# Kernel tuning notes

Hardware: AMD Instinct MI355X
Metric: run time of the kernel (lower is better)

Reference implementation:

```python
import jax, jax.numpy as jnp
import numpy as np

INPUT_SIZE = 1024
OUTPUT_SIZE = 1024
HEADS = 8
FREQ = 10000.0
NEG_INF = -1e9


def absolute_position(T, d, freq):
    # AP[p, 2i] = sin(p / freq^(2i/d)); AP[p, 2i+1] = cos(...). T assumed even.
    pos = jnp.arange(T, dtype=jnp.float32)[:, None]          # [T, 1]
    i = jnp.arange(T // 2, dtype=jnp.float32)[None, :]       # [1, T//2]
    angle = pos / (freq ** (2.0 * i / d))                    # [T, T//2]
    return jnp.stack([jnp.sin(angle), jnp.cos(angle)], axis=-1).reshape(T, T)


def setup_inputs() -> dict:
    key = jax.random.key(0)
    k_x, k_m, k_q, k_k, k_v, k_o = jax.random.split(key, 6)
    bs, n = 4, 2048
    dh = OUTPUT_SIZE // HEADS
    s_in = 1.0 / np.sqrt(INPUT_SIZE)
    s_out = 1.0 / np.sqrt(OUTPUT_SIZE)
    return {
        "x": jax.random.normal(k_x, (bs, n, INPUT_SIZE), dtype=jnp.float32),
        "mask": jax.random.randint(k_m, (bs, n), 0, 2, dtype=jnp.int32),
        # torch Linear weight layout: [out_features, in_features], stacked per head -> [H, dh, D]
        "Wq": jax.random.uniform(k_q, (HEADS, dh, INPUT_SIZE), jnp.float32, -s_in, s_in),
        "Wk": jax.random.uniform(k_k, (HEADS, dh, INPUT_SIZE), jnp.float32, -s_in, s_in),
        "Wv": jax.random.uniform(k_v, (HEADS, dh, INPUT_SIZE), jnp.float32, -s_in, s_in),
        "Wout": jax.random.uniform(k_o, (INPUT_SIZE, OUTPUT_SIZE), jnp.float32, -s_out, s_out),
    }


def reference(x, mask, Wq, Wk, Wv, Wout):
    bs, n, d = x.shape
    # per-head projections (no bias): [b, h, n, dh]
    Q = jnp.einsum('bnd,hed->bhne', x, Wq)
    K = jnp.einsum('bnd,hed->bhne', x, Wk)
    V = jnp.einsum('bnd,hed->bhne', x, Wv)
    # unscaled scores, as in the original module
    energies = jnp.einsum('bhqe,bhke->bhqk', Q, K)             # [b, h, n, n]
    AP = absolute_position(n, d, FREQ)                         # [n, n]
    energies = energies + AP
    m = mask.astype(bool)
    attn_mask = m[:, None, :, None] & m[:, None, None, :]      # [b, 1, n, n]
    energies = jnp.where(attn_mask, energies, NEG_INF)
    A = jax.nn.softmax(energies, axis=-1)                      # [b, h, n, n]
    # original computes (V^T @ A)^T == A^T @ V  (note transposed attention)
    y = jnp.einsum('bhji,bhje->bhie', A, V)                    # [b, h, n, dh]
    y = y.transpose(0, 2, 1, 3).reshape(bs, n, -1)             # concat heads -> [b, n, D]
    out = jnp.einsum('bnd,od->bno', y, Wout)
    return out, A[:, -1]  # original returns last head's att_weights
```

## Files before the change

### kernel.cpp

```cpp
#include <hip/hip_runtime.h>
#include <math.h>

#define BS_ 4
#define N_  2048
#define D_  1024
#define H_  8
#define DH_ 128

typedef __attribute__((ext_vector_type(8))) short short8;
typedef __attribute__((ext_vector_type(4))) short short4_t;
typedef __attribute__((ext_vector_type(4))) float float4_t;
typedef unsigned short u16;

__device__ __forceinline__ u16 f2bf(float f) {
    union { float f; unsigned u; } v; v.f = f;
    unsigned r = v.u + 0x7FFFu + ((v.u >> 16) & 1u);
    return (u16)(r >> 16);
}
__device__ __forceinline__ float bf2f(u16 h) {
    union { unsigned u; float f; } v; v.u = ((unsigned)h) << 16;
    return v.f;
}
__device__ __forceinline__ void split4(float a, float b, float c, float d,
                                       short4_t* hi, short4_t* lo) {
    u16 h0 = f2bf(a), h1 = f2bf(b), h2 = f2bf(c), h3 = f2bf(d);
    (*hi)[0] = (short)h0; (*hi)[1] = (short)h1; (*hi)[2] = (short)h2; (*hi)[3] = (short)h3;
    (*lo)[0] = (short)f2bf(a - bf2f(h0));
    (*lo)[1] = (short)f2bf(b - bf2f(h1));
    (*lo)[2] = (short)f2bf(c - bf2f(h2));
    (*lo)[3] = (short)f2bf(d - bf2f(h3));
}

__device__ __forceinline__ void gl_lds16(const void* g, void* l) {
    __builtin_amdgcn_global_load_lds(
        (const __attribute__((address_space(1))) unsigned int*)g,
        (__attribute__((address_space(3))) unsigned int*)l,
        16, 0, 0);
}

__global__ void apt_kernel(unsigned int* __restrict__ APtw) {
    int idx = blockIdx.x * 256 + threadIdx.x;
    int i = idx >> 10;
    int jw = idx & 1023;
    int u = i >> 1;
    float ex = exp2f(-(float)u * (13.287712379549449f / 512.0f));
    float a0 = (float)(2 * jw) * ex;
    float a1 = (float)(2 * jw + 1) * ex;
    float v0, v1;
    if (i & 1) { v0 = cosf(a0); v1 = cosf(a1); }
    else       { v0 = sinf(a0); v1 = sinf(a1); }
    APtw[(size_t)i * (N_ / 2) + jw] = (unsigned)f2bf(v0) | ((unsigned)f2bf(v1) << 16);
}

__global__ void split_kernel(const float* __restrict__ x,
                             const float* __restrict__ Wq, const float* __restrict__ Wk,
                             const float* __restrict__ Wv, const float* __restrict__ Wo,
                             u16* __restrict__ Xhi, u16* __restrict__ Xlo,
                             u16* __restrict__ Whi, u16* __restrict__ Wlo,
                             u16* __restrict__ Wvhi, u16* __restrict__ Wohi) {
    int i = blockIdx.x * 256 + threadIdx.x;
    const float* src; u16 *dhi, *dlo; size_t off;
    if (i < 2097152)      { src = x  + 4*(size_t)i;             dhi = Xhi;  dlo = Xlo;  off = 4*(size_t)i; }
    else if (i < 2359296) { size_t j = i - 2097152; src = Wq + 4*j; dhi = Whi; dlo = Wlo; off = 4*j; }
    else if (i < 2621440) { size_t j = i - 2359296; src = Wk + 4*j; dhi = Whi; dlo = Wlo; off = 1048576 + 4*j; }
    else if (i < 2883584) { size_t j = i - 2621440; src = Wv + 4*j; dhi = Wvhi; dlo = nullptr; off = 4*j; }
    else                  { size_t j = i - 2883584; src = Wo + 4*j; dhi = Wohi; dlo = nullptr; off = 4*j; }
    float4 v = *(const float4*)src;
    short4_t hi, lo;
    split4(v.x, v.y, v.z, v.w, &hi, &lo);
    *(short4_t*)(dhi + off) = hi;
    if (dlo) *(short4_t*)(dlo + off) = lo;
}

__global__ __launch_bounds__(256, 4) void qk_gemm(
    const u16* __restrict__ Xhi, const u16* __restrict__ Xlo,
    const u16* __restrict__ Whi, const u16* __restrict__ Wlo,
    u16* __restrict__ Qhi, u16* __restrict__ Qlo,
    u16* __restrict__ Khi, u16* __restrict__ Klo)
{
    const int mt = blockIdx.x;
    const int nt = blockIdx.y;
    const int tid = threadIdx.x, wave = tid >> 6, lane = tid & 63;
    const int quad = lane >> 4, l16 = lane & 15;

    __shared__ __align__(16) u16 sA[2][128 * 32];
    __shared__ __align__(16) u16 sB[2][128 * 32];

    const int srow = lane >> 2;
    const int scol = (lane & 3) * 8;
    const size_t aoff = ((size_t)(mt * 128) + srow) * 1024 + scol;
    const size_t boff = ((size_t)(nt * 128) + srow) * 1024 + scol;
    const int r0 = wave * 16, r1 = 64 + wave * 16;

    float4_t acc[2][8];
#pragma unroll
    for (int i = 0; i < 2; ++i)
#pragma unroll
        for (int j = 0; j < 8; ++j) acc[i][j] = (float4_t)(0.f);

    for (int kt = 0; kt < 32; ++kt) {
        __syncthreads();
        const int kc0 = kt * 32;
        gl_lds16(Xhi + aoff + (size_t)r0 * 1024 + kc0, &sA[0][r0 * 32]);
        gl_lds16(Xhi + aoff + (size_t)r1 * 1024 + kc0, &sA[0][r1 * 32]);
        gl_lds16(Xlo + aoff + (size_t)r0 * 1024 + kc0, &sA[1][r0 * 32]);
        gl_lds16(Xlo + aoff + (size_t)r1 * 1024 + kc0, &sA[1][r1 * 32]);
        gl_lds16(Whi + boff + (size_t)r0 * 1024 + kc0, &sB[0][r0 * 32]);
        gl_lds16(Whi + boff + (size_t)r1 * 1024 + kc0, &sB[0][r1 * 32]);
        gl_lds16(Wlo + boff + (size_t)r0 * 1024 + kc0, &sB[1][r0 * 32]);
        gl_lds16(Wlo + boff + (size_t)r1 * 1024 + kc0, &sB[1][r1 * 32]);
        __syncthreads();

#pragma unroll
        for (int t = 0; t < 3; ++t) {
            const u16* As = sA[t == 2 ? 1 : 0];
            const u16* Bs = sB[t == 1 ? 1 : 0];
            short8 afr[2];
#pragma unroll
            for (int mi = 0; mi < 2; ++mi)
                afr[mi] = *(const short8*)(As + (wave * 32 + mi * 16 + l16) * 32 + quad * 8);
#pragma unroll
            for (int ne = 0; ne < 8; ++ne) {
                short8 bfr = *(const short8*)(Bs + (ne * 16 + l16) * 32 + quad * 8);
#pragma unroll
                for (int mi = 0; mi < 2; ++mi)
                    acc[mi][ne] = __builtin_amdgcn_mfma_f32_16x16x32_bf16(afr[mi], bfr, acc[mi][ne], 0, 0, 0);
            }
        }
    }

    const int b = mt >> 4, q0 = (mt & 15) * 128;
    const bool isQ = (nt < 8);
    u16* Hi = isQ ? Qhi : Khi;
    u16* Lo = isQ ? Qlo : Klo;
    const int h = isQ ? nt : nt - 8;
    const size_t base = (size_t)(b * 8 + h) * N_ * DH_;
#pragma unroll
    for (int mi = 0; mi < 2; ++mi)
#pragma unroll
        for (int ne = 0; ne < 8; ++ne)
#pragma unroll
            for (int r = 0; r < 4; ++r) {
                int q = q0 + wave * 32 + mi * 16 + quad * 4 + r;
                int e = ne * 16 + l16;
                float v = acc[mi][ne][r];
                u16 hv = f2bf(v);
                Hi[base + (size_t)q * DH_ + e] = hv;
                Lo[base + (size_t)q * DH_ + e] = f2bf(v - bf2f(hv));
            }
}

__global__ __launch_bounds__(256, 4) void v_gemm(
    const u16* __restrict__ Wvhi, const u16* __restrict__ Xhi,
    u16* __restrict__ VT)
{
    const int qt = blockIdx.x;
    const int bh = blockIdx.y;
    const int b = bh >> 3, h = bh & 7;
    const int tid = threadIdx.x, wave = tid >> 6, lane = tid & 63;
    const int quad = lane >> 4, l16 = lane & 15;

    __shared__ __align__(16) u16 sA[128 * 32];
    __shared__ __align__(16) u16 sB[128 * 32];

    const int srow = lane >> 2, scol = (lane & 3) * 8;
    const size_t aoff = ((size_t)(h * 128) + srow) * 1024 + scol;
    const size_t boff = ((size_t)(b * N_ + qt * 128) + srow) * 1024 + scol;
    const int r0 = wave * 16, r1 = 64 + wave * 16;

    float4_t acc[2][8];
#pragma unroll
    for (int i = 0; i < 2; ++i)
#pragma unroll
        for (int j = 0; j < 8; ++j) acc[i][j] = (float4_t)(0.f);

    for (int kt = 0; kt < 32; ++kt) {
        __syncthreads();
        const int kc0 = kt * 32;
        gl_lds16(Wvhi + aoff + (size_t)r0 * 1024 + kc0, &sA[r0 * 32]);
        gl_lds16(Wvhi + aoff + (size_t)r1 * 1024 + kc0, &sA[r1 * 32]);
        gl_lds16(Xhi  + boff + (size_t)r0 * 1024 + kc0, &sB[r0 * 32]);
        gl_lds16(Xhi  + boff + (size_t)r1 * 1024 + kc0, &sB[r1 * 32]);
        __syncthreads();

        short8 afr[2];
#pragma unroll
        for (int mi = 0; mi < 2; ++mi)
            afr[mi] = *(const short8*)(sA + (wave * 32 + mi * 16 + l16) * 32 + quad * 8);
#pragma unroll
        for (int ne = 0; ne < 8; ++ne) {
            short8 bfr = *(const short8*)(sB + (ne * 16 + l16) * 32 + quad * 8);
#pragma unroll
            for (int mi = 0; mi < 2; ++mi)
                acc[mi][ne] = __builtin_amdgcn_mfma_f32_16x16x32_bf16(afr[mi], bfr, acc[mi][ne], 0, 0, 0);
        }
    }

    u16* Cg = VT + (size_t)bh * DH_ * N_;
#pragma unroll
    for (int mi = 0; mi < 2; ++mi)
#pragma unroll
        for (int ne = 0; ne < 8; ++ne)
#pragma unroll
            for (int r = 0; r < 4; ++r) {
                int e = wave * 32 + mi * 16 + quad * 4 + r;
                int q = qt * 128 + ne * 16 + l16;
                Cg[(size_t)e * N_ + q] = f2bf(acc[mi][ne][r]);
            }
}

__global__ __launch_bounds__(512, 4) void rowstats_kernel(
    const u16* __restrict__ Qhi, const u16* __restrict__ Qlo,
    const u16* __restrict__ Khi, const u16* __restrict__ Klo,
    const u16* __restrict__ APt,
    const int* __restrict__ mask,
    float* __restrict__ lrow)
{
    const int jt = blockIdx.x;
    const int bh = blockIdx.y;
    const int b = bh >> 3;
    const int tid = threadIdx.x, wave = tid >> 6, lane = tid & 63;
    const int quad = lane >> 4, l16 = lane & 15;
    const int jsub = (wave & 3) * 16, khalf = wave >> 2;

    __shared__ __align__(16) u16 ldsK[2][64 * 264];
    __shared__ int   s_mk[2][64];
    __shared__ float psum[64 * 2];

    short8 rQh[4], rQl[4];
    {
        const size_t qrow = ((size_t)bh * N_ + (size_t)(jt * 64 + jsub + l16)) * DH_;
#pragma unroll
        for (int kc = 0; kc < 4; ++kc) {
            rQh[kc] = *(const short8*)(Qhi + qrow + kc * 32 + quad * 8);
            rQl[kc] = *(const short8*)(Qlo + qrow + kc * 32 + quad * 8);
        }
    }

    const u16* ap_base = APt + (size_t)(khalf * 32 + l16) * N_ + jt * 64 + jsub + quad * 4;
    short4_t apc[2];
#pragma unroll
    for (int nk = 0; nk < 2; ++nk)
        apc[nk] = *(const short4_t*)(ap_base + (size_t)(nk * 16) * N_);

    {
        const size_t Kb = ((size_t)bh * N_) * DH_;
        for (int c = tid; c < 2048; c += 512) {
            int row = c >> 5, half = (c >> 4) & 1, seg = c & 15;
            *(short8*)(ldsK[0] + row * 264 + half * 128 + seg * 8) =
                *(const short8*)((half ? Klo : Khi) + Kb + (size_t)row * DH_ + seg * 8);
        }
        if (tid < 64) s_mk[0][tid] = mask[b * N_ + tid];
    }

    float p[4] = {0.f, 0.f, 0.f, 0.f};
    int mj_on[4];
#pragma unroll
    for (int r = 0; r < 4; ++r)
        mj_on[r] = mask[b * N_ + jt * 64 + jsub + quad * 4 + r];

    __syncthreads();

    for (int kt = 0; kt < 32; ++kt) {
        const int cur = kt & 1, nxt = cur ^ 1;
        short8 rK[4];
        short4_t apn[2];
        int rmk = 0;
        if (kt < 31) {
            const size_t Kb2 = ((size_t)bh * N_ + (size_t)(kt + 1) * 64) * DH_;
#pragma unroll
            for (int i = 0; i < 4; ++i) {
                int c = tid + i * 512;
                int row = c >> 5, half = (c >> 4) & 1, seg = c & 15;
                rK[i] = *(const short8*)((half ? Klo : Khi) + Kb2 + (size_t)row * DH_ + seg * 8);
            }
#pragma unroll
            for (int nk = 0; nk < 2; ++nk)
                apn[nk] = *(const short4_t*)(ap_base + (size_t)((kt + 1) * 64 + nk * 16) * N_);
            if (tid < 64) rmk = mask[b * N_ + (kt + 1) * 64 + tid];
        }

        float4_t acc[2];
        acc[0] = (float4_t)(0.f); acc[1] = (float4_t)(0.f);
#pragma unroll
        for (int kc = 0; kc < 4; ++kc) {
            short8 bH[2], bL[2];
#pragma unroll
            for (int nk = 0; nk < 2; ++nk)
                bH[nk] = *(const short8*)(ldsK[cur] + (khalf * 32 + nk * 16 + l16) * 264 + kc * 32 + quad * 8);
#pragma unroll
            for (int nk = 0; nk < 2; ++nk)
                acc[nk] = __builtin_amdgcn_mfma_f32_16x16x32_bf16(rQh[kc], bH[nk], acc[nk], 0, 0, 0);
#pragma unroll
            for (int nk = 0; nk < 2; ++nk)
                acc[nk] = __builtin_amdgcn_mfma_f32_16x16x32_bf16(rQl[kc], bH[nk], acc[nk], 0, 0, 0);
#pragma unroll
            for (int nk = 0; nk < 2; ++nk)
                bL[nk] = *(const short8*)(ldsK[cur] + (khalf * 32 + nk * 16 + l16) * 264 + 128 + kc * 32 + quad * 8);
#pragma unroll
            for (int nk = 0; nk < 2; ++nk)
                acc[nk] = __builtin_amdgcn_mfma_f32_16x16x32_bf16(rQh[kc], bL[nk], acc[nk], 0, 0, 0);
        }

#pragma unroll
        for (int nk = 0; nk < 2; ++nk) {
            int kk = khalf * 32 + nk * 16 + l16;
            int mk = s_mk[cur][kk];
#pragma unroll
            for (int r = 0; r < 4; ++r) {
                float e = acc[nk][r] + bf2f((u16)apc[nk][r]);
                e = (mj_on[r] && mk) ? e : -1.0e9f;
                p[r] += __expf(e);
            }
        }

        if (kt < 31) {
#pragma unroll
            for (int i = 0; i < 4; ++i) {
                int c = tid + i * 512;
                int row = c >> 5, half = (c >> 4) & 1, seg = c & 15;
                *(short8*)(ldsK[nxt] + row * 264 + half * 128 + seg * 8) = rK[i];
            }
            if (tid < 64) s_mk[nxt][tid] = rmk;
            apc[0] = apn[0]; apc[1] = apn[1];
        }
        __syncthreads();
    }

#pragma unroll
    for (int r = 0; r < 4; ++r) {
        float s = p[r];
        for (int off = 1; off < 16; off <<= 1)
            s += __shfl_xor(s, off, 64);
        if (l16 == 0)
            psum[(jsub + quad * 4 + r) * 2 + khalf] = s;
    }
    __syncthreads();
    if (tid < 64)
        lrow[(size_t)bh * N_ + jt * 64 + tid] = psum[tid * 2] + psum[tid * 2 + 1];
}

__global__ __launch_bounds__(512, 3) void attn_kernel(
    const u16* __restrict__ Qhi, const u16* __restrict__ Qlo,
    const u16* __restrict__ Khi, const u16* __restrict__ Klo,
    const u16* __restrict__ VT,
    const u16* __restrict__ APt,
    const int* __restrict__ mask,
    const float* __restrict__ lrow,
    u16* __restrict__ yout,
    float* __restrict__ aout)
{
    const int it = blockIdx.x;
    const int bh = blockIdx.y;
    const int b = bh >> 3, h = bh & 7;
    const int tid = threadIdx.x, wave = tid >> 6, lane = tid & 63;
    const int quad = lane >> 4, l16 = lane & 15;

    __shared__ __align__(16) u16 ldsQ[2][32 * 264];
    __shared__ __align__(16) u16 ldsV[2][128 * 32];
    __shared__ __align__(16) u16 ldsA[128 * 40];
    __shared__ __align__(16) float s_g[2][32];

    const int iq = wave & 3, jh = wave >> 2;
    const int igv0 = it * 128 + iq * 32 + l16;
    const int igv1 = igv0 + 16;

    short8 rKh[4][2], rKl[4][2];
    {
        const size_t kr0 = ((size_t)bh * N_ + igv0) * DH_;
        const size_t kr1 = ((size_t)bh * N_ + igv1) * DH_;
#pragma unroll
        for (int kc = 0; kc < 4; ++kc) {
            rKh[kc][0] = *(const short8*)(Khi + kr0 + kc * 32 + quad * 8);
            rKh[kc][1] = *(const short8*)(Khi + kr1 + kc * 32 + quad * 8);
            rKl[kc][0] = *(const short8*)(Klo + kr0 + kc * 32 + quad * 8);
            rKl[kc][1] = *(const short8*)(Klo + kr1 + kc * 32 + quad * 8);
        }
    }

    const u16* apb0 = APt + (size_t)igv0 * N_ + jh * 16 + quad * 4;
    const u16* apb1 = APt + (size_t)igv1 * N_ + jh * 16 + quad * 4;
    short4_t apc[2];
    apc[0] = *(const short4_t*)(apb0);
    apc[1] = *(const short4_t*)(apb1);

    const int ion0 = mask[b * N_ + igv0];
    const int ion1 = mask[b * N_ + igv1];

    {
        const size_t Qb0 = ((size_t)bh * N_) * DH_;
        for (int c = tid; c < 1024; c += 512) {
            int row = c >> 5, half = (c >> 4) & 1, seg = c & 15;
            *(short8*)(ldsQ[0] + row * 264 + half * 128 + seg * 8) =
                *(const short8*)((half ? Qlo : Qhi) + Qb0 + (size_t)row * DH_ + seg * 8);
        }
        { int e = tid >> 2, seg = tid & 3;
          gl_lds16(VT + (size_t)bh * DH_ * N_ + (size_t)e * N_ + seg * 8,
                   &ldsV[0][wave * 512]); }
        if (tid < 32) {
            float l = lrow[(size_t)bh * N_ + tid];
            int mj = mask[b * N_ + tid];
            s_g[0][tid] = (mj && l > 0.f) ? 1.0f / l : -1.0f;
        }
    }

    const int ip = wave >> 1, eh = wave & 1;

    float4_t accy[2][4];
#pragma unroll
    for (int ni = 0; ni < 2; ++ni)
#pragma unroll
        for (int ne = 0; ne < 4; ++ne) accy[ni][ne] = (float4_t)(0.f);

    const bool do_aout = (h == 7);
    const float inv_n = 1.0f / (float)N_;

    __syncthreads();

    for (int jt = 0; jt < 64; ++jt) {
        const int cur = jt & 1, nxt = cur ^ 1;
        const int j0 = jt * 32;

        short8 rQ[2];
        short4_t apn[2];
        float r_g = 0.f;
        if (jt < 63) {
            const int j0n = j0 + 32;
            { int e = tid >> 2, seg = tid & 3;
              gl_lds16(VT + (size_t)bh * DH_ * N_ + (size_t)e * N_ + j0n + seg * 8,
                       &ldsV[nxt][wave * 512]); }
            const size_t Qb2 = ((size_t)bh * N_ + j0n) * DH_;
#pragma unroll
            for (int i = 0; i < 2; ++i) {
                int c = tid + i * 512;
                int row = c >> 5, half = (c >> 4) & 1, seg = c & 15;
                rQ[i] = *(const short8*)((half ? Qlo : Qhi) + Qb2 + (size_t)row * DH_ + seg * 8);
            }
            apn[0] = *(const short4_t*)(apb0 + j0n);
            apn[1] = *(const short4_t*)(apb1 + j0n);
            if (tid < 32) {
                float l = lrow[(size_t)bh * N_ + j0n + tid];
                int mj = mask[b * N_ + j0n + tid];
                r_g = (mj && l > 0.f) ? 1.0f / l : -1.0f;
            }
        }

        float4_t accs[2];
        accs[0] = (float4_t)(0.f); accs[1] = (float4_t)(0.f);
        const u16* qbase = ldsQ[cur] + (jh * 16 + l16) * 264 + quad * 8;
#pragma unroll
        for (int kc = 0; kc < 4; ++kc) {
            short8 aH = *(const short8*)(qbase + kc * 32);
            accs[0] = __builtin_amdgcn_mfma_f32_16x16x32_bf16(aH, rKh[kc][0], accs[0], 0, 0, 0);
            accs[1] = __builtin_amdgcn_mfma_f32_16x16x32_bf16(aH, rKh[kc][1], accs[1], 0, 0, 0);
            short8 aL = *(const short8*)(qbase + 128 + kc * 32);
            accs[0] = __builtin_amdgcn_mfma_f32_16x16x32_bf16(aL, rKh[kc][0], accs[0], 0, 0, 0);
            accs[1] = __builtin_amdgcn_mfma_f32_16x16x32_bf16(aL, rKh[kc][1], accs[1], 0, 0, 0);
            accs[0] = __builtin_amdgcn_mfma_f32_16x16x32_bf16(aH, rKl[kc][0], accs[0], 0, 0, 0);
            accs[1] = __builtin_amdgcn_mfma_f32_16x16x32_bf16(aH, rKl[kc][1], accs[1], 0, 0, 0);
        }

        {
            float4_t g4 = *(const float4_t*)(&s_g[cur][jh * 16 + quad * 4]);
#pragma unroll
            for (int ih = 0; ih < 2; ++ih) {
                const int ig = ih ? igv1 : igv0;
                const int ion = ih ? ion1 : ion0;
                short4_t pk;
#pragma unroll
                for (int r = 0; r < 4; ++r) {
                    int jl = jh * 16 + quad * 4 + r;
                    float e = accs[ih][r] + bf2f((u16)apc[ih][r]);
                    float g = g4[r];
                    float a = (g < 0.f) ? inv_n : (ion ? __expf(e) * g : 0.f);
                    pk[r] = (short)f2bf(a);
                    if (do_aout)
                        aout[((size_t)(b * N_ + j0 + jl)) * N_ + ig] = a;
                }
                *(short4_t*)(ldsA + (size_t)(iq * 32 + ih * 16 + l16) * 40 + jh * 16 + quad * 4) = pk;
            }
        }
        __syncthreads();

        {
            short8 afrA[2];
#pragma unroll
            for (int ni = 0; ni < 2; ++ni)
                afrA[ni] = *(const short8*)(ldsA + (ip * 32 + ni * 16 + l16) * 40 + quad * 8);
#pragma unroll
            for (int ne = 0; ne < 4; ++ne) {
                short8 bfr = *(const short8*)(ldsV[cur] + (eh * 64 + ne * 16 + l16) * 32 + quad * 8);
#pragma unroll
                for (int ni = 0; ni < 2; ++ni)
                    accy[ni][ne] = __builtin_amdgcn_mfma_f32_16x16x32_bf16(afrA[ni], bfr, accy[ni][ne], 0, 0, 0);
            }
        }

        if (jt < 63) {
#pragma unroll
            for (int i = 0; i < 2; ++i) {
                int c = tid + i * 512;
                int row = c >> 5, half = (c >> 4) & 1, seg = c & 15;
                *(short8*)(ldsQ[nxt] + row * 264 + half * 128 + seg * 8) = rQ[i];
            }
            if (tid < 32) s_g[nxt][tid] = r_g;
            apc[0] = apn[0]; apc[1] = apn[1];
        }
        __syncthreads();
    }

#pragma unroll
    for (int ni = 0; ni < 2; ++ni)
#pragma unroll
        for (int ne = 0; ne < 4; ++ne)
#pragma unroll
            for (int r = 0; r < 4; ++r) {
                int irow = ip * 32 + ni * 16 + quad * 4 + r;
                int e = eh * 64 + ne * 16 + l16;
                yout[((size_t)b * N_ + it * 128 + irow) * D_ + h * DH_ + e] =
                    f2bf(accy[ni][ne][r]);
            }
}

__global__ __launch_bounds__(256, 4) void outgemm_kernel(
    const u16* __restrict__ A,
    const u16* __restrict__ B,
    float* __restrict__ C)
{
    const int nt = blockIdx.x;
    const int mt = blockIdx.y;
    const int tid = threadIdx.x, wave = tid >> 6, lane = tid & 63;
    const int quad = lane >> 4, l16 = lane & 15;

    __shared__ __align__(16) u16 sA[128 * 32];
    __shared__ __align__(16) u16 sB[128 * 32];

    const int srow = lane >> 2, scol = (lane & 3) * 8;
    const size_t aoff = ((size_t)(mt * 128) + srow) * 1024 + scol;
    const size_t boff = ((size_t)(nt * 128) + srow) * 1024 + scol;
    const int r0 = wave * 16, r1 = 64 + wave * 16;

    float4_t acc[2][8];
#pragma unroll
    for (int i = 0; i < 2; ++i)
#pragma unroll
        for (int j = 0; j < 8; ++j) acc[i][j] = (float4_t)(0.f);

    for (int kt = 0; kt < 32; ++kt) {
        __syncthreads();
        const int kc0 = kt * 32;
        gl_lds16(A + aoff + (size_t)r0 * 1024 + kc0, &sA[r0 * 32]);
        gl_lds16(A + aoff + (size_t)r1 * 1024 + kc0, &sA[r1 * 32]);
        gl_lds16(B + boff + (size_t)r0 * 1024 + kc0, &sB[r0 * 32]);
        gl_lds16(B + boff + (size_t)r1 * 1024 + kc0, &sB[r1 * 32]);
        __syncthreads();

        short8 afr[2];
#pragma unroll
        for (int mi = 0; mi < 2; ++mi)
            afr[mi] = *(const short8*)(sA + (wave * 32 + mi * 16 + l16) * 32 + quad * 8);
#pragma unroll
        for (int ne = 0; ne < 8; ++ne) {
            short8 bfr = *(const short8*)(sB + (ne * 16 + l16) * 32 + quad * 8);
#pragma unroll
            for (int mi = 0; mi < 2; ++mi)
                acc[mi][ne] = __builtin_amdgcn_mfma_f32_16x16x32_bf16(afr[mi], bfr, acc[mi][ne], 0, 0, 0);
        }
    }

#pragma unroll
    for (int mi = 0; mi < 2; ++mi)
#pragma unroll
        for (int ne = 0; ne < 8; ++ne)
#pragma unroll
            for (int r = 0; r < 4; ++r) {
                int row = mt * 128 + wave * 32 + mi * 16 + quad * 4 + r;
                int col = nt * 128 + ne * 16 + l16;
                C[(size_t)row * D_ + col] = acc[mi][ne][r];
            }
}

extern "C" void kernel_launch(void* const* d_in, const int* in_sizes, int n_in,
                              void* d_out, int out_size, void* d_ws, size_t ws_size,
                              hipStream_t stream)
{
    const float* x   = (const float*)d_in[0];
    const int*   msk = (const int*)d_in[1];
    const float* Wq  = (const float*)d_in[2];
    const float* Wk  = (const float*)d_in[3];
    const float* Wv  = (const float*)d_in[4];
    const float* Wo  = (const float*)d_in[5];

    float* out  = (float*)d_out;
    float* aout = out + (size_t)BS_ * N_ * D_;

    u16* Whi  = (u16*)d_out;
    u16* Wlo  = Whi  + (size_t)2048 * 1024;
    u16* Wvhi = Wlo  + (size_t)2048 * 1024;
    u16* Xhi  = Wvhi + (size_t)1024 * 1024;
    u16* Xlo  = Xhi  + (size_t)8192 * 1024;

    char* w = (char*)d_ws;
    u16* APt = (u16*)w;                       w += (size_t)N_ * N_ * 2;
    const size_t szqk = (size_t)BS_ * H_ * N_ * DH_ * 2;
    u16* Qhi = (u16*)w; w += szqk;
    u16* Qlo = (u16*)w; w += szqk;
    u16* Khi = (u16*)w; w += szqk;
    u16* Klo = (u16*)w; w += szqk;
    u16* VT  = (u16*)w; w += szqk;
    float* lrow = (float*)w;                  w += (size_t)BS_ * H_ * N_ * 4;
    u16* Wohi = (u16*)w;                      w += (size_t)D_ * D_ * 2;
    u16* yb   = (u16*)w;                      w += (size_t)BS_ * N_ * D_ * 2;

    apt_kernel<<<8192, 256, 0, stream>>>((unsigned int*)APt);
    split_kernel<<<12288, 256, 0, stream>>>(x, Wq, Wk, Wv, Wo,
                                            Xhi, Xlo, Whi, Wlo, Wvhi, Wohi);
    qk_gemm<<<dim3(64, 16), 256, 0, stream>>>(Xhi, Xlo, Whi, Wlo,
                                              Qhi, Qlo, Khi, Klo);
    v_gemm<<<dim3(16, 32), 256, 0, stream>>>(Wvhi, Xhi, VT);
    rowstats_kernel<<<dim3(32, 32), 512, 0, stream>>>(Qhi, Qlo, Khi, Klo, APt, msk, lrow);
    attn_kernel<<<dim3(16, 32), 512, 0, stream>>>(Qhi, Qlo, Khi, Klo, VT, APt, msk,
                                                  lrow, yb, aout);
    outgemm_kernel<<<dim3(8, 64), 256, 0, stream>>>(yb, Wohi, out);
}
```

Before: 673.6 us.

## Widen attention j-tile to 64, swizzle V LDS, split accumulators, raise MFMA priority

```diff
diff --git a/kernel.cpp b/kernel.cpp
--- a/kernel.cpp
+++ b/kernel.cpp
@@ -280,27 +280,36 @@
             if (tid < 64) rmk = mask[b * N_ + (kt + 1) * 64 + tid];
         }
 
-        float4_t acc[2];
-        acc[0] = (float4_t)(0.f); acc[1] = (float4_t)(0.f);
+        float4_t accA[2][2];
+#pragma unroll
+        for (int hf = 0; hf < 2; ++hf) {
+            accA[hf][0] = (float4_t)(0.f); accA[hf][1] = (float4_t)(0.f);
+        }
+        __builtin_amdgcn_s_setprio(1);
 #pragma unroll
         for (int kc = 0; kc < 4; ++kc) {
+            const int hf = kc >> 1;
             short8 bH[2], bL[2];
 #pragma unroll
             for (int nk = 0; nk < 2; ++nk)
                 bH[nk] = *(const short8*)(ldsK[cur] + (khalf * 32 + nk * 16 + l16) * 264 + kc * 32 + quad * 8);
 #pragma unroll
             for (int nk = 0; nk < 2; ++nk)
-                acc[nk] = __builtin_amdgcn_mfma_f32_16x16x32_bf16(rQh[kc], bH[nk], acc[nk], 0, 0, 0);
+                accA[hf][nk] = __builtin_amdgcn_mfma_f32_16x16x32_bf16(rQh[kc], bH[nk], accA[hf][nk], 0, 0, 0);
 #pragma unroll
             for (int nk = 0; nk < 2; ++nk)
-                acc[nk] = __builtin_amdgcn_mfma_f32_16x16x32_bf16(rQl[kc], bH[nk], acc[nk], 0, 0, 0);
+                accA[hf][nk] = __builtin_amdgcn_mfma_f32_16x16x32_bf16(rQl[kc], bH[nk], accA[hf][nk], 0, 0, 0);
 #pragma unroll
             for (int nk = 0; nk < 2; ++nk)
                 bL[nk] = *(const short8*)(ldsK[cur] + (khalf * 32 + nk * 16 + l16) * 264 + 128 + kc * 32 + quad * 8);
 #pragma unroll
             for (int nk = 0; nk < 2; ++nk)
-                acc[nk] = __builtin_amdgcn_mfma_f32_16x16x32_bf16(rQh[kc], bL[nk], acc[nk], 0, 0, 0);
-        }
+                accA[hf][nk] = __builtin_amdgcn_mfma_f32_16x16x32_bf16(rQh[kc], bL[nk], accA[hf][nk], 0, 0, 0);
+        }
+        __builtin_amdgcn_s_setprio(0);
+        float4_t acc[2];
+        acc[0] = accA[0][0] + accA[1][0];
+        acc[1] = accA[0][1] + accA[1][1];
 
 #pragma unroll
         for (int nk = 0; nk < 2; ++nk) {
@@ -340,7 +349,7 @@
         lrow[(size_t)bh * N_ + jt * 64 + tid] = psum[tid * 2] + psum[tid * 2 + 1];
 }
 
-__global__ __launch_bounds__(512, 3) void attn_kernel(
+__global__ __launch_bounds__(512, 2) void attn_kernel(
     const u16* __restrict__ Qhi, const u16* __restrict__ Qlo,
     const u16* __restrict__ Khi, const u16* __restrict__ Klo,
     const u16* __restrict__ VT,
@@ -356,14 +365,15 @@
     const int tid = threadIdx.x, wave = tid >> 6, lane = tid & 63;
     const int quad = lane >> 4, l16 = lane & 15;
 
-    __shared__ __align__(16) u16 ldsQ[2][32 * 264];
-    __shared__ __align__(16) u16 ldsV[2][128 * 32];
-    __shared__ __align__(16) u16 ldsA[128 * 40];
-    __shared__ __align__(16) float s_g[2][32];
-
-    const int iq = wave & 3, jh = wave >> 2;
+    __shared__ __align__(16) u16 ldsQ[2][64 * 264];
+    __shared__ __align__(16) u16 ldsV[2][128 * 64];
+    __shared__ __align__(16) u16 ldsA[128 * 72];
+    __shared__ __align__(16) float s_g[2][64];
+
+    const int iq = wave >> 1, jh = wave & 1;
     const int igv0 = it * 128 + iq * 32 + l16;
     const int igv1 = igv0 + 16;
+    const size_t vbase = (size_t)bh * DH_ * N_;
 
     short8 rKh[4][2], rKl[4][2];
     {
@@ -378,34 +388,39 @@
         }
     }
 
-    const u16* apb0 = APt + (size_t)igv0 * N_ + jh * 16 + quad * 4;
-    const u16* apb1 = APt + (size_t)igv1 * N_ + jh * 16 + quad * 4;
-    short4_t apc[2];
-    apc[0] = *(const short4_t*)(apb0);
-    apc[1] = *(const short4_t*)(apb1);
+    const u16* apb0 = APt + (size_t)igv0 * N_ + jh * 32 + quad * 4;
+    const u16* apb1 = APt + (size_t)igv1 * N_ + jh * 32 + quad * 4;
+    short4_t apc[2][2];
+#pragma unroll
+    for (int mj = 0; mj < 2; ++mj) {
+        apc[0][mj] = *(const short4_t*)(apb0 + mj * 16);
+        apc[1][mj] = *(const short4_t*)(apb1 + mj * 16);
+    }
 
     const int ion0 = mask[b * N_ + igv0];
     const int ion1 = mask[b * N_ + igv1];
 
     {
         const size_t Qb0 = ((size_t)bh * N_) * DH_;
-        for (int c = tid; c < 1024; c += 512) {
+        for (int c = tid; c < 2048; c += 512) {
             int row = c >> 5, half = (c >> 4) & 1, seg = c & 15;
             *(short8*)(ldsQ[0] + row * 264 + half * 128 + seg * 8) =
                 *(const short8*)((half ? Qlo : Qhi) + Qb0 + (size_t)row * DH_ + seg * 8);
         }
-        { int e = tid >> 2, seg = tid & 3;
-          gl_lds16(VT + (size_t)bh * DH_ * N_ + (size_t)e * N_ + seg * 8,
-                   &ldsV[0][wave * 512]); }
-        if (tid < 32) {
+#pragma unroll
+        for (int i = 0; i < 2; ++i) {
+            int c = i * 512 + wave * 64 + lane;
+            int e = c >> 3, g = c & 7;
+            gl_lds16(VT + vbase + (size_t)e * N_ + ((g ^ (e & 7)) * 8),
+                     ldsV[0] + (size_t)(i * 512 + wave * 64) * 8);
+        }
+        if (tid < 64) {
             float l = lrow[(size_t)bh * N_ + tid];
             int mj = mask[b * N_ + tid];
             s_g[0][tid] = (mj && l > 0.f) ? 1.0f / l : -1.0f;
         }
     }
 
-    const int ip = wave >> 1, eh = wave & 1;
-
     float4_t accy[2][4];
 #pragma unroll
     for (int ni = 0; ni < 2; ++ni)
@@ -417,94 +432,137 @@
 
     __syncthreads();
 
-    for (int jt = 0; jt < 64; ++jt) {
+    for (int jt = 0; jt < 32; ++jt) {
         const int cur = jt & 1, nxt = cur ^ 1;
-        const int j0 = jt * 32;
-
-        short8 rQ[2];
-        short4_t apn[2];
+        const int j0 = jt * 64;
+
+        short8 rQ[4];
+        short4_t apn[2][2];
         float r_g = 0.f;
-        if (jt < 63) {
-            const int j0n = j0 + 32;
-            { int e = tid >> 2, seg = tid & 3;
-              gl_lds16(VT + (size_t)bh * DH_ * N_ + (size_t)e * N_ + j0n + seg * 8,
-                       &ldsV[nxt][wave * 512]); }
+        if (jt < 31) {
+            const int j0n = j0 + 64;
+#pragma unroll
+            for (int i = 0; i < 2; ++i) {
+                int c = i * 512 + wave * 64 + lane;
+                int e = c >> 3, g = c & 7;
+                gl_lds16(VT + vbase + (size_t)e * N_ + j0n + ((g ^ (e & 7)) * 8),
+                         ldsV[nxt] + (size_t)(i * 512 + wave * 64) * 8);
+            }
             const size_t Qb2 = ((size_t)bh * N_ + j0n) * DH_;
 #pragma unroll
-            for (int i = 0; i < 2; ++i) {
+            for (int i = 0; i < 4; ++i) {
                 int c = tid + i * 512;
                 int row = c >> 5, half = (c >> 4) & 1, seg = c & 15;
                 rQ[i] = *(const short8*)((half ? Qlo : Qhi) + Qb2 + (size_t)row * DH_ + seg * 8);
             }
-            apn[0] = *(const short4_t*)(apb0 + j0n);
-            apn[1] = *(const short4_t*)(apb1 + j0n);
-            if (tid < 32) {
+#pragma unroll
+            for (int mj = 0; mj < 2; ++mj) {
+                apn[0][mj] = *(const short4_t*)(apb0 + j0n + mj * 16);
+                apn[1][mj] = *(const short4_t*)(apb1 + j0n + mj * 16);
+            }
+            if (tid < 64) {
                 float l = lrow[(size_t)bh * N_ + j0n + tid];
                 int mj = mask[b * N_ + j0n + tid];
                 r_g = (mj && l > 0.f) ? 1.0f / l : -1.0f;
             }
         }
 
-        float4_t accs[2];
-        accs[0] = (float4_t)(0.f); accs[1] = (float4_t)(0.f);
-        const u16* qbase = ldsQ[cur] + (jh * 16 + l16) * 264 + quad * 8;
+        float4_t accsA[2][2][2];
+#pragma unroll
+        for (int hf = 0; hf < 2; ++hf)
+#pragma unroll
+            for (int mj = 0; mj < 2; ++mj)
+#pragma unroll
+                for (int ih = 0; ih < 2; ++ih) accsA[hf][mj][ih] = (float4_t)(0.f);
+
+        __builtin_amdgcn_s_setprio(1);
 #pragma unroll
         for (int kc = 0; kc < 4; ++kc) {
-            short8 aH = *(const short8*)(qbase + kc * 32);
-            accs[0] = __builtin_amdgcn_mfma_f32_16x16x32_bf16(aH, rKh[kc][0], accs[0], 0, 0, 0);
-            accs[1] = __builtin_amdgcn_mfma_f32_16x16x32_bf16(aH, rKh[kc][1], accs[1], 0, 0, 0);
-            short8 aL = *(const short8*)(qbase + 128 + kc * 32);
-            accs[0] = __builtin_amdgcn_mfma_f32_16x16x32_bf16(aL, rKh[kc][0], accs[0], 0, 0, 0);
-            accs[1] = __builtin_amdgcn_mfma_f32_16x16x32_bf16(aL, rKh[kc][1], accs[1], 0, 0, 0);
-            accs[0] = __builtin_amdgcn_mfma_f32_16x16x32_bf16(aH, rKl[kc][0], accs[0], 0, 0, 0);
-            accs[1] = __builtin_amdgcn_mfma_f32_16x16x32_bf16(aH, rKl[kc][1], accs[1], 0, 0, 0);
-        }
-
-        {
-            float4_t g4 = *(const float4_t*)(&s_g[cur][jh * 16 + quad * 4]);
+            const int hf = kc >> 1;
+            short8 aH[2], aL[2];
+#pragma unroll
+            for (int mj = 0; mj < 2; ++mj)
+                aH[mj] = *(const short8*)(ldsQ[cur] + (jh * 32 + mj * 16 + l16) * 264 + kc * 32 + quad * 8);
+#pragma unroll
+            for (int mj = 0; mj < 2; ++mj)
+#pragma unroll
+                for (int ih = 0; ih < 2; ++ih)
+                    accsA[hf][mj][ih] = __builtin_amdgcn_mfma_f32_16x16x32_bf16(aH[mj], rKh[kc][ih], accsA[hf][mj][ih], 0, 0, 0);
+#pragma unroll
+            for (int mj = 0; mj < 2; ++mj)
+                aL[mj] = *(const short8*)(ldsQ[cur] + (jh * 32 + mj * 16 + l16) * 264 + 128 + kc * 32 + quad * 8);
+#pragma unroll
+            for (int mj = 0; mj < 2; ++mj)
+#pragma unroll
+                for (int ih = 0; ih < 2; ++ih)
+                    accsA[hf][mj][ih] = __builtin_amdgcn_mfma_f32_16x16x32_bf16(aL[mj], rKh[kc][ih], accsA[hf][mj][ih], 0, 0, 0);
+#pragma unroll
+            for (int mj = 0; mj < 2; ++mj)
+#pragma unroll
+                for (int ih = 0; ih < 2; ++ih)
+                    accsA[hf][mj][ih] = __builtin_amdgcn_mfma_f32_16x16x32_bf16(aH[mj], rKl[kc][ih], accsA[hf][mj][ih], 0, 0, 0);
+        }
+        __builtin_amdgcn_s_setprio(0);
+
+#pragma unroll
+        for (int mj = 0; mj < 2; ++mj) {
+            float4_t g4 = *(const float4_t*)(&s_g[cur][jh * 32 + mj * 16 + quad * 4]);
 #pragma unroll
             for (int ih = 0; ih < 2; ++ih) {
+                float4_t accs = accsA[0][mj][ih] + accsA[1][mj][ih];
                 const int ig = ih ? igv1 : igv0;
                 const int ion = ih ? ion1 : ion0;
                 short4_t pk;
 #pragma unroll
                 for (int r = 0; r < 4; ++r) {
-                    int jl = jh * 16 + quad * 4 + r;
-                    float e = accs[ih][r] + bf2f((u16)apc[ih][r]);
+                    int jl = jh * 32 + mj * 16 + quad * 4 + r;
+                    float e = accs[r] + bf2f((u16)apc[ih][mj][r]);
                     float g = g4[r];
                     float a = (g < 0.f) ? inv_n : (ion ? __expf(e) * g : 0.f);
                     pk[r] = (short)f2bf(a);
                     if (do_aout)
                         aout[((size_t)(b * N_ + j0 + jl)) * N_ + ig] = a;
                 }
-                *(short4_t*)(ldsA + (size_t)(iq * 32 + ih * 16 + l16) * 40 + jh * 16 + quad * 4) = pk;
+                *(short4_t*)(ldsA + (size_t)(iq * 32 + ih * 16 + l16) * 72 + jh * 32 + mj * 16 + quad * 4) = pk;
             }
         }
         __syncthreads();
 
         {
-            short8 afrA[2];
+            short8 afrA[2][2];
 #pragma unroll
             for (int ni = 0; ni < 2; ++ni)
-                afrA[ni] = *(const short8*)(ldsA + (ip * 32 + ni * 16 + l16) * 40 + quad * 8);
+#pragma unroll
+                for (int ks = 0; ks < 2; ++ks)
+                    afrA[ni][ks] = *(const short8*)(ldsA + (iq * 32 + ni * 16 + l16) * 72 + ks * 32 + quad * 8);
+            __builtin_amdgcn_s_setprio(1);
 #pragma unroll
             for (int ne = 0; ne < 4; ++ne) {
-                short8 bfr = *(const short8*)(ldsV[cur] + (eh * 64 + ne * 16 + l16) * 32 + quad * 8);
-#pragma unroll
-                for (int ni = 0; ni < 2; ++ni)
-                    accy[ni][ne] = __builtin_amdgcn_mfma_f32_16x16x32_bf16(afrA[ni], bfr, accy[ni][ne], 0, 0, 0);
-            }
-        }
-
-        if (jt < 63) {
-#pragma unroll
-            for (int i = 0; i < 2; ++i) {
+#pragma unroll
+                for (int ks = 0; ks < 2; ++ks) {
+                    short8 bfr = *(const short8*)(ldsV[cur] + (size_t)(jh * 64 + ne * 16 + l16) * 64 +
+                                                  (((ks * 4 + quad) ^ (l16 & 7)) * 8));
+#pragma unroll
+                    for (int ni = 0; ni < 2; ++ni)
+                        accy[ni][ne] = __builtin_amdgcn_mfma_f32_16x16x32_bf16(afrA[ni][ks], bfr, accy[ni][ne], 0, 0, 0);
+                }
+            }
+            __builtin_amdgcn_s_setprio(0);
+        }
+
+        if (jt < 31) {
+#pragma unroll
+            for (int i = 0; i < 4; ++i) {
                 int c = tid + i * 512;
                 int row = c >> 5, half = (c >> 4) & 1, seg = c & 15;
                 *(short8*)(ldsQ[nxt] + row * 264 + half * 128 + seg * 8) = rQ[i];
             }
-            if (tid < 32) s_g[nxt][tid] = r_g;
-            apc[0] = apn[0]; apc[1] = apn[1];
+            if (tid < 64) s_g[nxt][tid] = r_g;
+#pragma unroll
+            for (int mj = 0; mj < 2; ++mj) {
+                apc[0][mj] = apn[0][mj];
+                apc[1][mj] = apn[1][mj];
+            }
         }
         __syncthreads();
     }
@@ -515,8 +573,8 @@
         for (int ne = 0; ne < 4; ++ne)
 #pragma unroll
             for (int r = 0; r < 4; ++r) {
-                int irow = ip * 32 + ni * 16 + quad * 4 + r;
-                int e = eh * 64 + ne * 16 + l16;
+                int irow = iq * 32 + ni * 16 + quad * 4 + r;
+                int e = jh * 64 + ne * 16 + l16;
                 yout[((size_t)b * N_ + it * 128 + irow) * D_ + h * DH_ + e] =
                     f2bf(accy[ni][ne][r]);
             }
```

Result: faster. 638.0 us (-5.3%).
